# Kernel optimization log

Hardware: AMD Instinct MI355X
Metric: run time of the kernel (lower is better)

Reference implementation:

```python
import jax, jax.numpy as jnp
import numpy as np

N_SIN = 3  # fcn_n_sin (static)


def setup_inputs() -> dict:
    key = jax.random.key(0)
    ks = jax.random.split(key, 5)
    B, I, O, H = 256, 128, 128, 32
    F = 1 + 2 * N_SIN
    return {
        "x": jax.random.normal(ks[0], (B, I), dtype=jnp.float32),
        "W1": jax.random.normal(ks[1], (I, O, H, F), dtype=jnp.float32) * 0.3,
        "W2": jax.random.normal(ks[2], (I, O, 1, H), dtype=jnp.float32) * 0.3,
        "B1": jax.random.normal(ks[3], (I, O, H), dtype=jnp.float32) * 0.1,
        "B2": jax.random.normal(ks[4], (I, O, 1), dtype=jnp.float32) * 0.1,
    }


def reference(x, W1, W2, B1, B2):
    # x: [B, I]; per-(i,o) edge MLP on a scalar input, summed over i.
    omega = (2.0 ** jnp.arange(N_SIN)).astype(x.dtype)          # [S]
    ox = x[..., None] * omega                                    # [B, I, S]
    feat = jnp.concatenate([x[..., None], jnp.sin(ox), jnp.cos(ox)], axis=-1)  # [B, I, 1+2S]
    # First linear: per-edge [F -> H]
    h = jnp.einsum('bif,iohf->bioh', feat, W1) + B1              # [B, I, O, H]
    h = jax.nn.silu(h)
    # Second linear: per-edge [H -> 1], then sum over input dims i
    out = jnp.einsum('bioh,ioh->bio', h, W2[:, :, 0, :]) + B2[:, :, 0]  # [B, I, O]
    return out.sum(axis=1)                                       # [B, O]
```

## Files before the change

### kernel.cpp

```cpp
#include <hip/hip_runtime.h>
#include <hip/hip_bf16.h>

#define B_DIM 256
#define I_DIM 128
#define O_DIM 128
#define H_DIM 32
#define F_DIM 7
#define ICHUNK 8
#define NCHUNK (I_DIM / ICHUNK)
#define NLOG2E -1.4426950408889634f
#define NLN2   -0.6931471805599453f

typedef __attribute__((ext_vector_type(8))) short short8;
typedef __attribute__((ext_vector_type(4))) float float4v;
typedef __attribute__((ext_vector_type(2))) float float2v;

__device__ inline short bf16s(float v) {
    union { __hip_bfloat16 h; short s; } u;
    u.h = __float2bfloat16(v);
    return u.s;
}

__device__ inline float exp2_fast(float u) {
#if __has_builtin(__builtin_amdgcn_exp2f)
    return __builtin_amdgcn_exp2f(u);
#else
    return exp2f(u);
#endif
}

__device__ inline short8 feat_pack(float xv) {
    float s1 = __sinf(xv), c1 = __cosf(xv);
    float s2 = 2.f * s1 * c1, c2 = 1.f - 2.f * s1 * s1;
    float s4 = 2.f * s2 * c2, c4 = 1.f - 2.f * s2 * s2;
    short8 a;
    a[0] = bf16s(xv); a[1] = bf16s(s1); a[2] = bf16s(s2); a[3] = bf16s(s4);
    a[4] = bf16s(c1); a[5] = bf16s(c2); a[6] = bf16s(c4); a[7] = 0;
    return a;
}

__global__ __launch_bounds__(256)
void feat_kernel(const float* __restrict__ x, short* __restrict__ feat_g) {
    const int i = blockIdx.x;
    const int b = threadIdx.x;
    float xv = x[(size_t)b * I_DIM + i];
    *reinterpret_cast<short8*>(feat_g + ((size_t)i * B_DIM + b) * 8) = feat_pack(xv);
}

__global__ __launch_bounds__(128, 8)
void fcnkan_ws(const short* __restrict__ feat_g,
               const float* __restrict__ W1,
               const float* __restrict__ W2,
               const float* __restrict__ B1,
               const float* __restrict__ B2,
               float* __restrict__ ws) {
    __shared__ __align__(16) short w1_s[ICHUNK * H_DIM * 8];
    __shared__ float b1_s[ICHUNK * H_DIM];
    __shared__ float w2_s[ICHUNK * H_DIM];

    const int tid  = threadIdx.x;
    const int o    = blockIdx.x;
    const int ic0  = blockIdx.y * ICHUNK;
    const int bh   = blockIdx.z;
    const int w    = tid >> 6;
    const int lane = tid & 63;
    const int m    = lane & 15;
    const int q    = lane >> 4;
    const int brow = bh * 128 + w * 64;

    const short8 zero8 = {};

    #pragma unroll
    for (int s = 0; s < 2; ++s) {
        int idx = s * 128 + tid;
        int il = idx >> 5, h = idx & 31;
        size_t iobase = (size_t)(ic0 + il) * O_DIM + o;
        const float* wr = W1 + iobase * (H_DIM * F_DIM) + h * F_DIM;
        short8 bfr;
        #pragma unroll
        for (int f = 0; f < F_DIM; ++f) bfr[f] = bf16s(wr[f] * NLOG2E);
        bfr[7] = 0;
        *reinterpret_cast<short8*>(w1_s + idx * 8) = bfr;
        b1_s[idx] = B1[iobase * H_DIM + h] * NLOG2E;
        w2_s[idx] = W2[iobase * H_DIM + h] * NLN2;
    }
    __syncthreads();

    float2v acc2[8];
    #pragma unroll
    for (int p = 0; p < 8; ++p) acc2[p] = (float2v){0.f, 0.f};

    #pragma unroll 1
    for (int il = 0; il < ICHUNK; ++il) {
        const short8* fG = reinterpret_cast<const short8*>(feat_g)
                           + (size_t)(ic0 + il) * B_DIM;
        const short8* wS = reinterpret_cast<const short8*>(w1_s) + il * H_DIM;

        short8 afrag[4];
        #pragma unroll
        for (int t = 0; t < 4; ++t)
            afrag[t] = fG[brow + t * 16 + m];

        short8 bfrag[2];
        float  b1v[2], w2v[2];
        #pragma unroll
        for (int nt = 0; nt < 2; ++nt) {
            int h = nt * 16 + m;
            short8 b = wS[h];
            bfrag[nt] = (q == 0) ? b : zero8;
            b1v[nt] = b1_s[il * H_DIM + h];
            w2v[nt] = w2_s[il * H_DIM + h];
        }

        #pragma unroll
        for (int nt = 0; nt < 2; ++nt) {
            float4v c0 = {b1v[nt], b1v[nt], b1v[nt], b1v[nt]};
            float2v w2p = {w2v[nt], w2v[nt]};
            #pragma unroll
            for (int t = 0; t < 4; ++t) {
                float4v z = __builtin_amdgcn_mfma_f32_16x16x32_bf16(
                    afrag[t], bfrag[nt], c0, 0, 0, 0);
                #pragma unroll
                for (int r = 0; r < 4; r += 2) {
                    float2v u = {z[r], z[r + 1]};
                    float2v e = {exp2_fast(u.x), exp2_fast(u.y)};
                    float2v s = e + 1.f;
                    float2v sg = {__builtin_amdgcn_rcpf(s.x),
                                  __builtin_amdgcn_rcpf(s.y)};
                    float2v p = u * sg;
                    acc2[t * 2 + (r >> 1)] = p * w2p + acc2[t * 2 + (r >> 1)];
                }
            }
        }
    }

    float acc[16];
    #pragma unroll
    for (int t = 0; t < 4; ++t) {
        acc[t * 4 + 0] = acc2[t * 2 + 0].x;
        acc[t * 4 + 1] = acc2[t * 2 + 0].y;
        acc[t * 4 + 2] = acc2[t * 2 + 1].x;
        acc[t * 4 + 3] = acc2[t * 2 + 1].y;
    }
    #pragma unroll
    for (int r = 0; r < 16; ++r) {
        float v = acc[r];
        v += __shfl_xor(v, 1, 64);
        v += __shfl_xor(v, 2, 64);
        v += __shfl_xor(v, 4, 64);
        v += __shfl_xor(v, 8, 64);
        acc[r] = v;
    }

    float b2c = 0.f;
    for (int il = 0; il < ICHUNK; ++il) b2c += B2[(size_t)(ic0 + il) * O_DIM + o];

    if (m == 0) {
        float* wsp = ws + ((size_t)blockIdx.y * O_DIM + o) * B_DIM;
        #pragma unroll
        for (int t = 0; t < 4; ++t)
            #pragma unroll
            for (int r = 0; r < 4; ++r)
                wsp[brow + t * 16 + q * 4 + r] = acc[t * 4 + r] + b2c;
    }
}

__global__ __launch_bounds__(256)
void reduce_kernel(const float* __restrict__ ws, float* __restrict__ out) {
    const int o = blockIdx.x;
    const int b = threadIdx.x;
    float s = 0.f;
    #pragma unroll
    for (int c = 0; c < NCHUNK; ++c)
        s += ws[((size_t)c * O_DIM + o) * B_DIM + b];
    out[(size_t)b * O_DIM + o] = s;
}

__global__ __launch_bounds__(256, 2)
void fcnkan_atomic(const float* __restrict__ x,
                   const float* __restrict__ W1,
                   const float* __restrict__ W2,
                   const float* __restrict__ B1,
                   const float* __restrict__ B2,
                   float* __restrict__ out) {
    __shared__ __align__(16) short feat_s[ICHUNK * B_DIM * 8];
    __shared__ __align__(16) short w1_s[ICHUNK * H_DIM * 8];
    __shared__ float b1_s[ICHUNK * H_DIM];
    __shared__ float w2_s[ICHUNK * H_DIM];

    const int tid  = threadIdx.x;
    const int o    = blockIdx.x;
    const int ic0  = blockIdx.y * ICHUNK;
    const int w    = tid >> 6;
    const int lane = tid & 63;
    const int m    = lane & 15;
    const int q    = lane >> 4;

    const short8 zero8 = {};

    {
        const float4* xp = reinterpret_cast<const float4*>(x + (size_t)tid * I_DIM + ic0);
        float4 x0 = xp[0], x1 = xp[1];
        float xr[8] = {x0.x, x0.y, x0.z, x0.w, x1.x, x1.y, x1.z, x1.w};
        #pragma unroll
        for (int il = 0; il < ICHUNK; ++il)
            *reinterpret_cast<short8*>(feat_s + (il * B_DIM + tid) * 8) = feat_pack(xr[il]);
    }
    {
        int il = tid >> 5, h = tid & 31;
        size_t iobase = (size_t)(ic0 + il) * O_DIM + o;
        const float* wr = W1 + iobase * (H_DIM * F_DIM) + h * F_DIM;
        short8 bfr;
        #pragma unroll
        for (int f = 0; f < F_DIM; ++f) bfr[f] = bf16s(wr[f]);
        bfr[7] = 0;
        *reinterpret_cast<short8*>(w1_s + tid * 8) = bfr;
        b1_s[tid] = B1[iobase * H_DIM + h];
        w2_s[tid] = W2[iobase * H_DIM + h];
    }
    __syncthreads();

    float acc[16];
    #pragma unroll
    for (int r = 0; r < 16; ++r) acc[r] = 0.f;

    #pragma unroll 1
    for (int il = 0; il < ICHUNK; ++il) {
        const short8* fS = reinterpret_cast<const short8*>(feat_s) + il * B_DIM;
        const short8* wS = reinterpret_cast<const short8*>(w1_s) + il * H_DIM;

        short8 afrag[4];
        #pragma unroll
        for (int t = 0; t < 4; ++t)
            afrag[t] = fS[w * 64 + t * 16 + m];

        short8 bfrag[2];
        float  b1v[2], w2v[2];
        #pragma unroll
        for (int nt = 0; nt < 2; ++nt) {
            int h = nt * 16 + m;
            short8 b = wS[h];
            bfrag[nt] = (q == 0) ? b : zero8;
            b1v[nt] = b1_s[il * H_DIM + h];
            w2v[nt] = w2_s[il * H_DIM + h];
        }

        #pragma unroll
        for (int nt = 0; nt < 2; ++nt) {
            float4v c0 = {b1v[nt], b1v[nt], b1v[nt], b1v[nt]};
            #pragma unroll
            for (int t = 0; t < 4; ++t) {
                float4v z = __builtin_amdgcn_mfma_f32_16x16x32_bf16(
                    afrag[t], bfrag[nt], c0, 0, 0, 0);
                #pragma unroll
                for (int r = 0; r < 4; ++r) {
                    float zz = z[r];
                    float sg = __builtin_amdgcn_rcpf(1.f + __expf(-zz));
                    acc[t * 4 + r] = fmaf(zz * sg, w2v[nt], acc[t * 4 + r]);
                }
            }
        }
    }

    #pragma unroll
    for (int r = 0; r < 16; ++r) {
        float v = acc[r];
        v += __shfl_xor(v, 1, 64);
        v += __shfl_xor(v, 2, 64);
        v += __shfl_xor(v, 4, 64);
        v += __shfl_xor(v, 8, 64);
        acc[r] = v;
    }

    float b2c = 0.f;
    for (int il = 0; il < ICHUNK; ++il) b2c += B2[(size_t)(ic0 + il) * O_DIM + o];

    if (m == 0) {
        #pragma unroll
        for (int t = 0; t < 4; ++t)
            #pragma unroll
            for (int r = 0; r < 4; ++r) {
                int b = w * 64 + t * 16 + q * 4 + r;
                atomicAdd(&out[(size_t)b * O_DIM + o], acc[t * 4 + r] + b2c);
            }
    }
}

extern "C" void kernel_launch(void* const* d_in, const int* in_sizes, int n_in,
                              void* d_out, int out_size, void* d_ws, size_t ws_size,
                              hipStream_t stream) {
    const float* x  = (const float*)d_in[0];
    const float* W1 = (const float*)d_in[1];
    const float* W2 = (const float*)d_in[2];
    const float* B1 = (const float*)d_in[3];
    const float* B2 = (const float*)d_in[4];
    float* out = (float*)d_out;
    float* ws  = (float*)d_ws;

    const size_t part_bytes = (size_t)NCHUNK * O_DIM * B_DIM * sizeof(float);
    const size_t feat_bytes = (size_t)I_DIM * B_DIM * 8 * sizeof(short);
    const size_t ws_need = part_bytes + feat_bytes;

    if (ws_size >= ws_need) {
        short* feat_g = (short*)((char*)d_ws + part_bytes);
        feat_kernel<<<I_DIM, B_DIM, 0, stream>>>(x, feat_g);
        dim3 grid(O_DIM, NCHUNK, 2);
        fcnkan_ws<<<grid, 128, 0, stream>>>(feat_g, W1, W2, B1, B2, ws);
        reduce_kernel<<<O_DIM, B_DIM, 0, stream>>>(ws, out);
    } else {
        hipMemsetAsync(out, 0, (size_t)out_size * sizeof(float), stream);
        dim3 grid(O_DIM, NCHUNK);
        fcnkan_atomic<<<grid, 256, 0, stream>>>(x, W1, W2, B1, B2, out);
    }
}
```

Measured before the change: 105.3 us.

## Fuse feature computation into main kernel via per-block LDS recompute

Removes the separate feature kernel and its global workspace buffer. Each block now loads its slice of x, computes the sin/cos bf16 features into shared memory and reads A fragments from LDS instead of global memory. This saves a kernel launch and the global round-trip, at the cost of redundant feature computation across output blocks, 16KB more LDS per block and a lower occupancy hint.

```diff
diff --git a/kernel.cpp b/kernel.cpp
--- a/kernel.cpp
+++ b/kernel.cpp
@@ -39,21 +39,14 @@
     return a;
 }
 
-__global__ __launch_bounds__(256)
-void feat_kernel(const float* __restrict__ x, short* __restrict__ feat_g) {
-    const int i = blockIdx.x;
-    const int b = threadIdx.x;
-    float xv = x[(size_t)b * I_DIM + i];
-    *reinterpret_cast<short8*>(feat_g + ((size_t)i * B_DIM + b) * 8) = feat_pack(xv);
-}
-
-__global__ __launch_bounds__(128, 8)
-void fcnkan_ws(const short* __restrict__ feat_g,
+__global__ __launch_bounds__(128, 4)
+void fcnkan_ws(const float* __restrict__ x,
                const float* __restrict__ W1,
                const float* __restrict__ W2,
                const float* __restrict__ B1,
                const float* __restrict__ B2,
                float* __restrict__ ws) {
+    __shared__ __align__(16) short feat_s[ICHUNK * 128 * 8];
     __shared__ __align__(16) short w1_s[ICHUNK * H_DIM * 8];
     __shared__ float b1_s[ICHUNK * H_DIM];
     __shared__ float w2_s[ICHUNK * H_DIM];
@@ -70,6 +63,17 @@
 
     const short8 zero8 = {};
 
+    {
+        const float4* xp = reinterpret_cast<const float4*>(
+            x + (size_t)(bh * 128 + tid) * I_DIM + ic0);
+        float4 x0 = xp[0], x1 = xp[1];
+        float xr[8] = {x0.x, x0.y, x0.z, x0.w, x1.x, x1.y, x1.z, x1.w};
+        #pragma unroll
+        for (int il = 0; il < ICHUNK; ++il)
+            *reinterpret_cast<short8*>(feat_s + (il * 128 + tid) * 8) =
+                feat_pack(xr[il]);
+    }
+
     #pragma unroll
     for (int s = 0; s < 2; ++s) {
         int idx = s * 128 + tid;
@@ -92,14 +96,13 @@
 
     #pragma unroll 1
     for (int il = 0; il < ICHUNK; ++il) {
-        const short8* fG = reinterpret_cast<const short8*>(feat_g)
-                           + (size_t)(ic0 + il) * B_DIM;
+        const short8* fS = reinterpret_cast<const short8*>(feat_s) + il * 128;
         const short8* wS = reinterpret_cast<const short8*>(w1_s) + il * H_DIM;
 
         short8 afrag[4];
         #pragma unroll
         for (int t = 0; t < 4; ++t)
-            afrag[t] = fG[brow + t * 16 + m];
+            afrag[t] = fS[w * 64 + t * 16 + m];
 
         short8 bfrag[2];
         float  b1v[2], w2v[2];
@@ -297,15 +300,11 @@
     float* out = (float*)d_out;
     float* ws  = (float*)d_ws;
 
-    const size_t part_bytes = (size_t)NCHUNK * O_DIM * B_DIM * sizeof(float);
-    const size_t feat_bytes = (size_t)I_DIM * B_DIM * 8 * sizeof(short);
-    const size_t ws_need = part_bytes + feat_bytes;
+    const size_t ws_need = (size_t)NCHUNK * O_DIM * B_DIM * sizeof(float);
 
     if (ws_size >= ws_need) {
-        short* feat_g = (short*)((char*)d_ws + part_bytes);
-        feat_kernel<<<I_DIM, B_DIM, 0, stream>>>(x, feat_g);
         dim3 grid(O_DIM, NCHUNK, 2);
-        fcnkan_ws<<<grid, 128, 0, stream>>>(feat_g, W1, W2, B1, B2, ws);
+        fcnkan_ws<<<grid, 128, 0, stream>>>(x, W1, W2, B1, B2, ws);
         reduce_kernel<<<O_DIM, B_DIM, 0, stream>>>(ws, out);
     } else {
         hipMemsetAsync(out, 0, (size_t)out_size * sizeof(float), stream);
```

Result: no change. 106.9 us (+1.5%).
